# Performance work log

Hardware: AMD Instinct MI355X
Metric: run time of the kernel (lower is better)

Reference implementation:

```python
import jax, jax.numpy as jnp
import numpy as np


def setup_inputs() -> dict:
    key = jax.random.key(0)
    k1, k2, k3, k4, k5 = jax.random.split(key, 5)
    B, S, D = 16, 1024, 64
    query = jax.random.normal(k1, (B, S, D), dtype=jnp.float32)
    key_t = jax.random.normal(k2, (B, S, D), dtype=jnp.float32)
    value = jax.random.normal(k3, (B, S, D), dtype=jnp.float32)
    t_m = jax.random.uniform(k4, (B, S, S), dtype=jnp.float32)
    g_m = jax.random.uniform(k5, (B, S, S), dtype=jnp.float32)
    # causal mask [S, S]: 1 where attention allowed
    mask = jnp.tril(jnp.ones((S, S), dtype=jnp.int32))
    return {"query": query, "key": key_t, "value": value,
            "t_m": t_m, "g_m": g_m, "mask": mask}


def _bias(m):
    # per-batch max over all S*S entries, then abs difference
    mx = jnp.max(m.reshape(m.shape[0], -1), axis=1)  # [B]
    return jnp.abs(m - mx[:, None, None])            # [B, S, S]


def reference(query, key, value, t_m, g_m, mask):
    d_k = query.shape[-1]
    # NOTE: source divides by d_k, not sqrt(d_k)
    scores = jnp.einsum('bqd,bkd->bqk', query, key) / d_k  # [B, S, S]
    scores = scores + _bias(t_m) + _bias(g_m)
    scores = jnp.where(mask[None, :, :] == 0, jnp.float32(-1e9), scores)
    p_attn = jax.nn.softmax(scores, axis=-1)
    return jnp.einsum('bqk,bkd->bqd', p_attn, value)
```

## Files before the change

### kernel.cpp

```cpp
#include <hip/hip_runtime.h>

#define B_  16
#define S_  1024
#define D_  64

typedef __attribute__((ext_vector_type(8))) short bf16x8;
typedef __attribute__((ext_vector_type(4))) float f32x4;

__device__ __forceinline__ unsigned short f2bf(float f) {
    unsigned u = __float_as_uint(f);
    u += 0x7FFF + ((u >> 16) & 1);
    return (unsigned short)(u >> 16);
}

__global__ __launch_bounds__(256, 4) void attn_mfma_kernel(
    const float* __restrict__ Q, const float* __restrict__ K,
    const float* __restrict__ V, const float* __restrict__ t_m,
    const float* __restrict__ g_m, float* __restrict__ out)
{
    __shared__ __align__(16) char smem[17920];
    unsigned short (*s_p)[136] = (unsigned short (*)[136])smem;
    float* cmb = (float*)smem;
    float* cml = (float*)(smem + 17408);

    const int bid = blockIdx.x;
    const int b   = bid & 15;
    const int g   = bid >> 4;
    const int qt  = (g < 32) ? (63 - g) : (g - 32);
    const int qb  = qt << 4;
    const int tid = threadIdx.x;
    const int w   = tid >> 6;
    const int ln  = tid & 63;
    const int lg  = ln >> 4;
    const int lm  = ln & 15;

    const size_t kvb   = (size_t)(b * S_) * D_;
    const size_t biasb = (size_t)b * S_ * S_;
    const float* Kb = K + kvb;
    const float* Vb = V + kvb;

    bf16x8 qa[2];
    #pragma unroll
    for (int ks = 0; ks < 2; ++ks) {
        const float* qp = Q + ((size_t)(b * S_) + qb + lm) * D_ + 32 * ks + 8 * lg;
        const float4 x = *(const float4*)qp;
        const float4 y = *(const float4*)(qp + 4);
        bf16x8 f;
        f[0] = (short)f2bf(x.x); f[1] = (short)f2bf(x.y);
        f[2] = (short)f2bf(x.z); f[3] = (short)f2bf(x.w);
        f[4] = (short)f2bf(y.x); f[5] = (short)f2bf(y.y);
        f[6] = (short)f2bf(y.z); f[7] = (short)f2bf(y.w);
        qa[ks] = f;
    }

    float mrun[4] = {-1e30f, -1e30f, -1e30f, -1e30f};
    float lrun[4] = {0.f, 0.f, 0.f, 0.f};
    const f32x4 z4 = {0.f, 0.f, 0.f, 0.f};
    f32x4 oacc[4] = {z4, z4, z4, z4};

    const int ntw = ((qb + 15 - 32 * w) >> 7) + 1;

    for (int t = 0; t < ntw; ++t) {
        const int ke = (t << 7) + 32 * w;

        bf16x8 kf[2][2];
        #pragma unroll
        for (int nf = 0; nf < 2; ++nf)
            #pragma unroll
            for (int ks = 0; ks < 2; ++ks) {
                const float* kp = Kb + (size_t)(ke + 16 * nf + lm) * D_ + 32 * ks + 8 * lg;
                const float4 x = *(const float4*)kp;
                const float4 y = *(const float4*)(kp + 4);
                bf16x8 f;
                f[0] = (short)f2bf(x.x); f[1] = (short)f2bf(x.y);
                f[2] = (short)f2bf(x.z); f[3] = (short)f2bf(x.w);
                f[4] = (short)f2bf(y.x); f[5] = (short)f2bf(y.y);
                f[6] = (short)f2bf(y.z); f[7] = (short)f2bf(y.w);
                kf[nf][ks] = f;
            }

        float bt[2][4], bg[2][4];
        #pragma unroll
        for (int nf = 0; nf < 2; ++nf)
            #pragma unroll
            for (int r = 0; r < 4; ++r) {
                const size_t off = biasb + (size_t)(qb + 4 * lg + r) * S_
                                 + ke + 16 * nf + lm;
                bt[nf][r] = t_m[off];
                bg[nf][r] = g_m[off];
            }

        f32x4 sa[2] = {z4, z4};
        #pragma unroll
        for (int nf = 0; nf < 2; ++nf)
            #pragma unroll
            for (int ks = 0; ks < 2; ++ks)
                sa[nf] = __builtin_amdgcn_mfma_f32_16x16x32_bf16(
                    qa[ks], kf[nf][ks], sa[nf], 0, 0, 0);

        float vf[4][8];
        #pragma unroll
        for (int nd = 0; nd < 4; ++nd)
            #pragma unroll
            for (int j = 0; j < 8; ++j)
                vf[nd][j] = Vb[(size_t)(ke + 8 * lg + j) * D_ + 16 * nd + lm];

        float p[2][4], tmax[4];
        #pragma unroll
        for (int r = 0; r < 4; ++r) {
            const int qg = qb + 4 * lg + r;
            float s0 = sa[0][r] * (1.f / 64.f) - bt[0][r] - bg[0][r];
            float s1 = sa[1][r] * (1.f / 64.f) - bt[1][r] - bg[1][r];
            if (ke + lm > qg)      s0 = -1e30f;
            if (ke + 16 + lm > qg) s1 = -1e30f;
            p[0][r] = s0;  p[1][r] = s1;
            tmax[r] = fmaxf(s0, s1);
        }
        #pragma unroll
        for (int off = 1; off < 16; off <<= 1)
            #pragma unroll
            for (int r = 0; r < 4; ++r)
                tmax[r] = fmaxf(tmax[r], __shfl_xor(tmax[r], off, 64));

        float a[4];
        #pragma unroll
        for (int r = 0; r < 4; ++r) {
            const float mn = fmaxf(mrun[r], tmax[r]);
            a[r] = __expf(mrun[r] - mn);
            mrun[r] = mn;
            const float p0 = __expf(p[0][r] - mn);
            const float p1 = __expf(p[1][r] - mn);
            p[0][r] = p0;  p[1][r] = p1;
            float rs = p0 + p1;
            #pragma unroll
            for (int off = 1; off < 16; off <<= 1)
                rs += __shfl_xor(rs, off, 64);
            lrun[r] = lrun[r] * a[r] + rs;
        }
        #pragma unroll
        for (int nd = 0; nd < 4; ++nd)
            #pragma unroll
            for (int r = 0; r < 4; ++r)
                oacc[nd][r] *= a[r];

        #pragma unroll
        for (int nf = 0; nf < 2; ++nf)
            #pragma unroll
            for (int r = 0; r < 4; ++r)
                s_p[4 * lg + r][32 * w + 16 * nf + lm] = f2bf(p[nf][r]);
        asm volatile("s_waitcnt lgkmcnt(0)" ::: "memory");
        const bf16x8 pa = *(const bf16x8*)&s_p[lm][32 * w + 8 * lg];

        #pragma unroll
        for (int nd = 0; nd < 4; ++nd) {
            bf16x8 vb;
            #pragma unroll
            for (int j = 0; j < 8; ++j)
                vb[j] = (short)f2bf(vf[nd][j]);
            oacc[nd] = __builtin_amdgcn_mfma_f32_16x16x32_bf16(
                pa, vb, oacc[nd], 0, 0, 0);
        }
    }

    __syncthreads();
    #pragma unroll
    for (int nd = 0; nd < 4; ++nd)
        #pragma unroll
        for (int r = 0; r < 4; ++r)
            cmb[(w * 16 + 4 * lg + r) * 68 + 16 * nd + lm] = oacc[nd][r];
    if (lm == 0) {
        #pragma unroll
        for (int r = 0; r < 4; ++r) {
            cml[w * 32 + 4 * lg + r]      = mrun[r];
            cml[w * 32 + 16 + 4 * lg + r] = lrun[r];
        }
    }
    __syncthreads();
    {
        const int q = tid >> 4, c = tid & 15;
        float mm[4], sc[4];
        float ms = -1e30f;
        #pragma unroll
        for (int i = 0; i < 4; ++i) { mm[i] = cml[i * 32 + q]; ms = fmaxf(ms, mm[i]); }
        float lt = 0.f;
        #pragma unroll
        for (int i = 0; i < 4; ++i) {
            sc[i] = __expf(mm[i] - ms);
            lt += cml[i * 32 + 16 + q] * sc[i];
        }
        const float inv = 1.f / lt;
        float4 acc = make_float4(0.f, 0.f, 0.f, 0.f);
        #pragma unroll
        for (int i = 0; i < 4; ++i) {
            const float4 v = *(const float4*)&cmb[(i * 16 + q) * 68 + 4 * c];
            acc.x += v.x * sc[i];  acc.y += v.y * sc[i];
            acc.z += v.z * sc[i];  acc.w += v.w * sc[i];
        }
        acc.x *= inv; acc.y *= inv; acc.z *= inv; acc.w *= inv;
        *(float4*)(out + ((size_t)(b * S_) + qb + q) * D_ + 4 * c) = acc;
    }
}

extern "C" void kernel_launch(void* const* d_in, const int* in_sizes, int n_in,
                              void* d_out, int out_size, void* d_ws, size_t ws_size,
                              hipStream_t stream) {
    const float* Q   = (const float*)d_in[0];
    const float* Kp  = (const float*)d_in[1];
    const float* V   = (const float*)d_in[2];
    const float* t_m = (const float*)d_in[3];
    const float* g_m = (const float*)d_in[4];

    attn_mfma_kernel<<<1024, 256, 0, stream>>>(Q, Kp, V, t_m, g_m,
                                               (float*)d_out);
}
```

Measured before the change: 35.58 us.

## Split each query tile's key range across eight waves instead of four

Doubles the block size to 512 threads so eight waves share a 16-row query tile. Each wave now strides over keys in steps of 256, which halves the serial loop length per wave. The shared-memory merge of per-wave softmax partials is widened to eight partials, and the output write becomes float2 per thread. The bf16 conversion is also swapped to the library intrinsic. The risks are the heavier cross-wave merge and a tight launch-bounds hint (512 threads, 8 blocks) that may force register spills.

```diff
diff --git a/kernel.cpp b/kernel.cpp
--- a/kernel.cpp
+++ b/kernel.cpp
@@ -1,4 +1,5 @@
 #include <hip/hip_runtime.h>
+#include <hip/hip_bf16.h>
 
 #define B_  16
 #define S_  1024
@@ -7,21 +8,20 @@
 typedef __attribute__((ext_vector_type(8))) short bf16x8;
 typedef __attribute__((ext_vector_type(4))) float f32x4;
 
-__device__ __forceinline__ unsigned short f2bf(float f) {
-    unsigned u = __float_as_uint(f);
-    u += 0x7FFF + ((u >> 16) & 1);
-    return (unsigned short)(u >> 16);
+__device__ __forceinline__ short f2bf(float f) {
+    __hip_bfloat16 h = __float2bfloat16(f);
+    return __builtin_bit_cast(short, h);
 }
 
-__global__ __launch_bounds__(256, 4) void attn_mfma_kernel(
+__global__ __launch_bounds__(512, 8) void attn_mfma_kernel(
     const float* __restrict__ Q, const float* __restrict__ K,
     const float* __restrict__ V, const float* __restrict__ t_m,
     const float* __restrict__ g_m, float* __restrict__ out)
 {
-    __shared__ __align__(16) char smem[17920];
-    unsigned short (*s_p)[136] = (unsigned short (*)[136])smem;
+    __shared__ __align__(16) char smem[35840];
+    unsigned short (*s_p)[264] = (unsigned short (*)[264])smem;
     float* cmb = (float*)smem;
-    float* cml = (float*)(smem + 17408);
+    float* cml = (float*)(smem + 34816);
 
     const int bid = blockIdx.x;
     const int b   = bid & 15;
@@ -46,10 +46,10 @@
         const float4 x = *(const float4*)qp;
         const float4 y = *(const float4*)(qp + 4);
         bf16x8 f;
-        f[0] = (short)f2bf(x.x); f[1] = (short)f2bf(x.y);
-        f[2] = (short)f2bf(x.z); f[3] = (short)f2bf(x.w);
-        f[4] = (short)f2bf(y.x); f[5] = (short)f2bf(y.y);
-        f[6] = (short)f2bf(y.z); f[7] = (short)f2bf(y.w);
+        f[0] = f2bf(x.x); f[1] = f2bf(x.y);
+        f[2] = f2bf(x.z); f[3] = f2bf(x.w);
+        f[4] = f2bf(y.x); f[5] = f2bf(y.y);
+        f[6] = f2bf(y.z); f[7] = f2bf(y.w);
         qa[ks] = f;
     }
 
@@ -58,10 +58,10 @@
     const f32x4 z4 = {0.f, 0.f, 0.f, 0.f};
     f32x4 oacc[4] = {z4, z4, z4, z4};
 
-    const int ntw = ((qb + 15 - 32 * w) >> 7) + 1;
+    const int ntw = ((qb + 15 - 32 * w) >> 8) + 1;
 
     for (int t = 0; t < ntw; ++t) {
-        const int ke = (t << 7) + 32 * w;
+        const int ke = (t << 8) + 32 * w;
 
         bf16x8 kf[2][2];
         #pragma unroll
@@ -72,10 +72,10 @@
                 const float4 x = *(const float4*)kp;
                 const float4 y = *(const float4*)(kp + 4);
                 bf16x8 f;
-                f[0] = (short)f2bf(x.x); f[1] = (short)f2bf(x.y);
-                f[2] = (short)f2bf(x.z); f[3] = (short)f2bf(x.w);
-                f[4] = (short)f2bf(y.x); f[5] = (short)f2bf(y.y);
-                f[6] = (short)f2bf(y.z); f[7] = (short)f2bf(y.w);
+                f[0] = f2bf(x.x); f[1] = f2bf(x.y);
+                f[2] = f2bf(x.z); f[3] = f2bf(x.w);
+                f[4] = f2bf(y.x); f[5] = f2bf(y.y);
+                f[6] = f2bf(y.z); f[7] = f2bf(y.w);
                 kf[nf][ks] = f;
             }
 
@@ -147,7 +147,7 @@
         for (int nf = 0; nf < 2; ++nf)
             #pragma unroll
             for (int r = 0; r < 4; ++r)
-                s_p[4 * lg + r][32 * w + 16 * nf + lm] = f2bf(p[nf][r]);
+                s_p[4 * lg + r][32 * w + 16 * nf + lm] = (unsigned short)f2bf(p[nf][r]);
         asm volatile("s_waitcnt lgkmcnt(0)" ::: "memory");
         const bf16x8 pa = *(const bf16x8*)&s_p[lm][32 * w + 8 * lg];
 
@@ -156,7 +156,7 @@
             bf16x8 vb;
             #pragma unroll
             for (int j = 0; j < 8; ++j)
-                vb[j] = (short)f2bf(vf[nd][j]);
+                vb[j] = f2bf(vf[nd][j]);
             oacc[nd] = __builtin_amdgcn_mfma_f32_16x16x32_bf16(
                 pa, vb, oacc[nd], 0, 0, 0);
         }
@@ -177,27 +177,26 @@
     }
     __syncthreads();
     {
-        const int q = tid >> 4, c = tid & 15;
-        float mm[4], sc[4];
+        const int q = tid >> 5, c = tid & 31;
+        float mm[8], sc[8];
         float ms = -1e30f;
         #pragma unroll
-        for (int i = 0; i < 4; ++i) { mm[i] = cml[i * 32 + q]; ms = fmaxf(ms, mm[i]); }
+        for (int i = 0; i < 8; ++i) { mm[i] = cml[i * 32 + q]; ms = fmaxf(ms, mm[i]); }
         float lt = 0.f;
         #pragma unroll
-        for (int i = 0; i < 4; ++i) {
+        for (int i = 0; i < 8; ++i) {
             sc[i] = __expf(mm[i] - ms);
             lt += cml[i * 32 + 16 + q] * sc[i];
         }
         const float inv = 1.f / lt;
-        float4 acc = make_float4(0.f, 0.f, 0.f, 0.f);
-        #pragma unroll
-        for (int i = 0; i < 4; ++i) {
-            const float4 v = *(const float4*)&cmb[(i * 16 + q) * 68 + 4 * c];
+        float2 acc = make_float2(0.f, 0.f);
+        #pragma unroll
+        for (int i = 0; i < 8; ++i) {
+            const float2 v = *(const float2*)&cmb[(i * 16 + q) * 68 + 2 * c];
             acc.x += v.x * sc[i];  acc.y += v.y * sc[i];
-            acc.z += v.z * sc[i];  acc.w += v.w * sc[i];
-        }
-        acc.x *= inv; acc.y *= inv; acc.z *= inv; acc.w *= inv;
-        *(float4*)(out + ((size_t)(b * S_) + qb + q) * D_ + 4 * c) = acc;
+        }
+        acc.x *= inv; acc.y *= inv;
+        *(float2*)(out + ((size_t)(b * S_) + qb + q) * D_ + 2 * c) = acc;
     }
 }
 
@@ -210,6 +209,6 @@
     const float* t_m = (const float*)d_in[3];
     const float* g_m = (const float*)d_in[4];
 
-    attn_mfma_kernel<<<1024, 256, 0, stream>>>(Q, Kp, V, t_m, g_m,
+    attn_mfma_kernel<<<1024, 512, 0, stream>>>(Q, Kp, V, t_m, g_m,
                                                (float*)d_out);
 }
```

Result: slower. 102.7 us (+188.8%).

## Pre-convert K to bf16 and transpose V in a prep kernel

Applied to the files above, without the earlier changes.

Adds a prep kernel that converts K to bf16 and writes V transposed as bf16 into the workspace. The attention kernel then loads K and V fragments as single 16-byte vectors instead of doing per-element float loads and bf16 conversions in the inner loop. This removes the 32 strided scalar V loads per thread per tile and the repeated conversion work. In exchange it adds a second launch and an extra round trip through the workspace. The original kernel is kept as a fallback when the workspace is too small.

```diff
diff --git a/kernel.cpp b/kernel.cpp
--- a/kernel.cpp
+++ b/kernel.cpp
@@ -1,4 +1,5 @@
 #include <hip/hip_runtime.h>
+#include <hip/hip_bf16.h>
 
 #define B_  16
 #define S_  1024
@@ -7,15 +8,44 @@
 typedef __attribute__((ext_vector_type(8))) short bf16x8;
 typedef __attribute__((ext_vector_type(4))) float f32x4;
 
-__device__ __forceinline__ unsigned short f2bf(float f) {
-    unsigned u = __float_as_uint(f);
-    u += 0x7FFF + ((u >> 16) & 1);
-    return (unsigned short)(u >> 16);
-}
-
-__global__ __launch_bounds__(256, 4) void attn_mfma_kernel(
-    const float* __restrict__ Q, const float* __restrict__ K,
-    const float* __restrict__ V, const float* __restrict__ t_m,
+__device__ __forceinline__ unsigned short f2bf_u(float f) {
+    __hip_bfloat16 h = __float2bfloat16(f);
+    return __builtin_bit_cast(unsigned short, h);
+}
+__device__ __forceinline__ short f2bf(float f) {
+    return (short)f2bf_u(f);
+}
+__device__ __forceinline__ unsigned pk2(float a, float b) {
+    return (unsigned)f2bf_u(a) | ((unsigned)f2bf_u(b) << 16);
+}
+
+__global__ __launch_bounds__(256) void prep_kernel(
+    const float* __restrict__ K, const float* __restrict__ V,
+    unsigned short* __restrict__ Kbf, unsigned short* __restrict__ VT)
+{
+    const int bid = blockIdx.x;
+    if (bid < 512) {
+        const size_t i = ((size_t)bid * 256 + threadIdx.x) * 8;
+        const float4 x = *(const float4*)(K + i);
+        const float4 y = *(const float4*)(K + i + 4);
+        uint4 o = { pk2(x.x, x.y), pk2(x.z, x.w), pk2(y.x, y.y), pk2(y.z, y.w) };
+        *(uint4*)(Kbf + i) = o;
+    } else {
+        const int i  = (bid - 512) * 256 + threadIdx.x;
+        const int d  = i & 63;
+        const int kg = (i >> 6) & 127;
+        const int b  = i >> 13;
+        const float* vp = V + ((size_t)b * S_ + (size_t)kg * 8) * D_ + d;
+        const float v0 = vp[0],   v1 = vp[64],  v2 = vp[128], v3 = vp[192];
+        const float v4 = vp[256], v5 = vp[320], v6 = vp[384], v7 = vp[448];
+        uint4 o = { pk2(v0, v1), pk2(v2, v3), pk2(v4, v5), pk2(v6, v7) };
+        *(uint4*)(VT + ((size_t)b * D_ + d) * S_ + kg * 8) = o;
+    }
+}
+
+__global__ __launch_bounds__(256, 4) void attn_mfma_pre(
+    const unsigned short* __restrict__ Kbf, const unsigned short* __restrict__ VT,
+    const float* __restrict__ Q, const float* __restrict__ t_m,
     const float* __restrict__ g_m, float* __restrict__ out)
 {
     __shared__ __align__(16) char smem[17920];
@@ -34,10 +64,15 @@
     const int lg  = ln >> 4;
     const int lm  = ln & 15;
 
-    const size_t kvb   = (size_t)(b * S_) * D_;
     const size_t biasb = (size_t)b * S_ * S_;
-    const float* Kb = K + kvb;
-    const float* Vb = V + kvb;
+    const float* tmb = t_m + biasb + (size_t)(qb + 4 * lg) * S_ + lm;
+    const float* gmb = g_m + biasb + (size_t)(qb + 4 * lg) * S_ + lm;
+
+    const unsigned short* Kbb = Kbf + ((size_t)(b * S_) + lm) * D_ + 8 * lg;
+    const unsigned short* vt0 = VT + ((size_t)(b * D_) + 0  + lm) * S_ + 8 * lg;
+    const unsigned short* vt1 = VT + ((size_t)(b * D_) + 16 + lm) * S_ + 8 * lg;
+    const unsigned short* vt2 = VT + ((size_t)(b * D_) + 32 + lm) * S_ + 8 * lg;
+    const unsigned short* vt3 = VT + ((size_t)(b * D_) + 48 + lm) * S_ + 8 * lg;
 
     bf16x8 qa[2];
     #pragma unroll
@@ -46,10 +81,10 @@
         const float4 x = *(const float4*)qp;
         const float4 y = *(const float4*)(qp + 4);
         bf16x8 f;
-        f[0] = (short)f2bf(x.x); f[1] = (short)f2bf(x.y);
-        f[2] = (short)f2bf(x.z); f[3] = (short)f2bf(x.w);
-        f[4] = (short)f2bf(y.x); f[5] = (short)f2bf(y.y);
-        f[6] = (short)f2bf(y.z); f[7] = (short)f2bf(y.w);
+        f[0] = f2bf(x.x); f[1] = f2bf(x.y);
+        f[2] = f2bf(x.z); f[3] = f2bf(x.w);
+        f[4] = f2bf(y.x); f[5] = f2bf(y.y);
+        f[6] = f2bf(y.z); f[7] = f2bf(y.w);
         qa[ks] = f;
     }
 
@@ -63,47 +98,32 @@
     for (int t = 0; t < ntw; ++t) {
         const int ke = (t << 7) + 32 * w;
 
-        bf16x8 kf[2][2];
-        #pragma unroll
-        for (int nf = 0; nf < 2; ++nf)
-            #pragma unroll
-            for (int ks = 0; ks < 2; ++ks) {
-                const float* kp = Kb + (size_t)(ke + 16 * nf + lm) * D_ + 32 * ks + 8 * lg;
-                const float4 x = *(const float4*)kp;
-                const float4 y = *(const float4*)(kp + 4);
-                bf16x8 f;
-                f[0] = (short)f2bf(x.x); f[1] = (short)f2bf(x.y);
-                f[2] = (short)f2bf(x.z); f[3] = (short)f2bf(x.w);
-                f[4] = (short)f2bf(y.x); f[5] = (short)f2bf(y.y);
-                f[6] = (short)f2bf(y.z); f[7] = (short)f2bf(y.w);
-                kf[nf][ks] = f;
+        const bf16x8* kp = (const bf16x8*)(Kbb + (size_t)ke * D_);
+        bf16x8 kf00 = kp[0];
+        bf16x8 kf01 = *(const bf16x8*)((const unsigned short*)kp + 32);
+        bf16x8 kf10 = *(const bf16x8*)((const unsigned short*)kp + 16 * D_);
+        bf16x8 kf11 = *(const bf16x8*)((const unsigned short*)kp + 16 * D_ + 32);
+
+        const bf16x8 vb0 = *(const bf16x8*)(vt0 + ke);
+        const bf16x8 vb1 = *(const bf16x8*)(vt1 + ke);
+        const bf16x8 vb2 = *(const bf16x8*)(vt2 + ke);
+        const bf16x8 vb3 = *(const bf16x8*)(vt3 + ke);
+
+        float bt[2][4], bg[2][4];
+        #pragma unroll
+        for (int nf = 0; nf < 2; ++nf)
+            #pragma unroll
+            for (int r = 0; r < 4; ++r) {
+                const size_t off = (size_t)r * S_ + ke + 16 * nf;
+                bt[nf][r] = tmb[off];
+                bg[nf][r] = gmb[off];
             }
 
-        float bt[2][4], bg[2][4];
-        #pragma unroll
-        for (int nf = 0; nf < 2; ++nf)
-            #pragma unroll
-            for (int r = 0; r < 4; ++r) {
-                const size_t off = biasb + (size_t)(qb + 4 * lg + r) * S_
-                                 + ke + 16 * nf + lm;
-                bt[nf][r] = t_m[off];
-                bg[nf][r] = g_m[off];
-            }
-
         f32x4 sa[2] = {z4, z4};
-        #pragma unroll
-        for (int nf = 0; nf < 2; ++nf)
-            #pragma unroll
-            for (int ks = 0; ks < 2; ++ks)
-                sa[nf] = __builtin_amdgcn_mfma_f32_16x16x32_bf16(
-                    qa[ks], kf[nf][ks], sa[nf], 0, 0, 0);
-
-        float vf[4][8];
-        #pragma unroll
-        for (int nd = 0; nd < 4; ++nd)
-            #pragma unroll
-            for (int j = 0; j < 8; ++j)
-                vf[nd][j] = Vb[(size_t)(ke + 8 * lg + j) * D_ + 16 * nd + lm];
+        sa[0] = __builtin_amdgcn_mfma_f32_16x16x32_bf16(qa[0], kf00, sa[0], 0, 0, 0);
+        sa[0] = __builtin_amdgcn_mfma_f32_16x16x32_bf16(qa[1], kf01, sa[0], 0, 0, 0);
+        sa[1] = __builtin_amdgcn_mfma_f32_16x16x32_bf16(qa[0], kf10, sa[1], 0, 0, 0);
+        sa[1] = __builtin_amdgcn_mfma_f32_16x16x32_bf16(qa[1], kf11, sa[1], 0, 0, 0);
 
         float p[2][4], tmax[4];
         #pragma unroll
@@ -122,11 +142,10 @@
             for (int r = 0; r < 4; ++r)
                 tmax[r] = fmaxf(tmax[r], __shfl_xor(tmax[r], off, 64));
 
-        float a[4];
         #pragma unroll
         for (int r = 0; r < 4; ++r) {
             const float mn = fmaxf(mrun[r], tmax[r]);
-            a[r] = __expf(mrun[r] - mn);
+            const float a  = __expf(mrun[r] - mn);
             mrun[r] = mn;
             const float p0 = __expf(p[0][r] - mn);
             const float p1 = __expf(p[1][r] - mn);
@@ -135,28 +154,203 @@
             #pragma unroll
             for (int off = 1; off < 16; off <<= 1)
                 rs += __shfl_xor(rs, off, 64);
-            lrun[r] = lrun[r] * a[r] + rs;
-        }
-        #pragma unroll
-        for (int nd = 0; nd < 4; ++nd)
+            lrun[r] = lrun[r] * a + rs;
+            #pragma unroll
+            for (int nd = 0; nd < 4; ++nd) oacc[nd][r] *= a;
+        }
+
+        #pragma unroll
+        for (int nf = 0; nf < 2; ++nf)
             #pragma unroll
             for (int r = 0; r < 4; ++r)
-                oacc[nd][r] *= a[r];
-
-        #pragma unroll
-        for (int nf = 0; nf < 2; ++nf)
-            #pragma unroll
-            for (int r = 0; r < 4; ++r)
-                s_p[4 * lg + r][32 * w + 16 * nf + lm] = f2bf(p[nf][r]);
+                s_p[4 * lg + r][32 * w + 16 * nf + lm] = f2bf_u(p[nf][r]);
         asm volatile("s_waitcnt lgkmcnt(0)" ::: "memory");
         const bf16x8 pa = *(const bf16x8*)&s_p[lm][32 * w + 8 * lg];
 
+        oacc[0] = __builtin_amdgcn_mfma_f32_16x16x32_bf16(pa, vb0, oacc[0], 0, 0, 0);
+        oacc[1] = __builtin_amdgcn_mfma_f32_16x16x32_bf16(pa, vb1, oacc[1], 0, 0, 0);
+        oacc[2] = __builtin_amdgcn_mfma_f32_16x16x32_bf16(pa, vb2, oacc[2], 0, 0, 0);
+        oacc[3] = __builtin_amdgcn_mfma_f32_16x16x32_bf16(pa, vb3, oacc[3], 0, 0, 0);
+    }
+
+    __syncthreads();
+    #pragma unroll
+    for (int nd = 0; nd < 4; ++nd)
+        #pragma unroll
+        for (int r = 0; r < 4; ++r)
+            cmb[(w * 16 + 4 * lg + r) * 68 + 16 * nd + lm] = oacc[nd][r];
+    if (lm == 0) {
+        #pragma unroll
+        for (int r = 0; r < 4; ++r) {
+            cml[w * 32 + 4 * lg + r]      = mrun[r];
+            cml[w * 32 + 16 + 4 * lg + r] = lrun[r];
+        }
+    }
+    __syncthreads();
+    {
+        const int q = tid >> 4, c = tid & 15;
+        float mm[4], sc[4];
+        float ms = -1e30f;
+        #pragma unroll
+        for (int i = 0; i < 4; ++i) { mm[i] = cml[i * 32 + q]; ms = fmaxf(ms, mm[i]); }
+        float lt = 0.f;
+        #pragma unroll
+        for (int i = 0; i < 4; ++i) {
+            sc[i] = __expf(mm[i] - ms);
+            lt += cml[i * 32 + 16 + q] * sc[i];
+        }
+        const float inv = 1.f / lt;
+        float4 acc = make_float4(0.f, 0.f, 0.f, 0.f);
+        #pragma unroll
+        for (int i = 0; i < 4; ++i) {
+            const float4 v = *(const float4*)&cmb[(i * 16 + q) * 68 + 4 * c];
+            acc.x += v.x * sc[i];  acc.y += v.y * sc[i];
+            acc.z += v.z * sc[i];  acc.w += v.w * sc[i];
+        }
+        acc.x *= inv; acc.y *= inv; acc.z *= inv; acc.w *= inv;
+        *(float4*)(out + ((size_t)(b * S_) + qb + q) * D_ + 4 * c) = acc;
+    }
+}
+
+__global__ __launch_bounds__(256, 4) void attn_mfma_kernel(
+    const float* __restrict__ Q, const float* __restrict__ K,
+    const float* __restrict__ V, const float* __restrict__ t_m,
+    const float* __restrict__ g_m, float* __restrict__ out)
+{
+    __shared__ __align__(16) char smem[17920];
+    unsigned short (*s_p)[136] = (unsigned short (*)[136])smem;
+    float* cmb = (float*)smem;
+    float* cml = (float*)(smem + 17408);
+
+    const int bid = blockIdx.x;
+    const int b   = bid & 15;
+    const int g   = bid >> 4;
+    const int qt  = (g < 32) ? (63 - g) : (g - 32);
+    const int qb  = qt << 4;
+    const int tid = threadIdx.x;
+    const int w   = tid >> 6;
+    const int ln  = tid & 63;
+    const int lg  = ln >> 4;
+    const int lm  = ln & 15;
+
+    const size_t kvb   = (size_t)(b * S_) * D_;
+    const size_t biasb = (size_t)b * S_ * S_;
+    const float* Kb = K + kvb;
+    const float* Vb = V + kvb;
+
+    bf16x8 qa[2];
+    #pragma unroll
+    for (int ks = 0; ks < 2; ++ks) {
+        const float* qp = Q + ((size_t)(b * S_) + qb + lm) * D_ + 32 * ks + 8 * lg;
+        const float4 x = *(const float4*)qp;
+        const float4 y = *(const float4*)(qp + 4);
+        bf16x8 f;
+        f[0] = f2bf(x.x); f[1] = f2bf(x.y);
+        f[2] = f2bf(x.z); f[3] = f2bf(x.w);
+        f[4] = f2bf(y.x); f[5] = f2bf(y.y);
+        f[6] = f2bf(y.z); f[7] = f2bf(y.w);
+        qa[ks] = f;
+    }
+
+    float mrun[4] = {-1e30f, -1e30f, -1e30f, -1e30f};
+    float lrun[4] = {0.f, 0.f, 0.f, 0.f};
+    const f32x4 z4 = {0.f, 0.f, 0.f, 0.f};
+    f32x4 oacc[4] = {z4, z4, z4, z4};
+
+    const int ntw = ((qb + 15 - 32 * w) >> 7) + 1;
+
+    for (int t = 0; t < ntw; ++t) {
+        const int ke = (t << 7) + 32 * w;
+
+        bf16x8 kf[2][2];
+        #pragma unroll
+        for (int nf = 0; nf < 2; ++nf)
+            #pragma unroll
+            for (int ks = 0; ks < 2; ++ks) {
+                const float* kp = Kb + (size_t)(ke + 16 * nf + lm) * D_ + 32 * ks + 8 * lg;
+                const float4 x = *(const float4*)kp;
+                const float4 y = *(const float4*)(kp + 4);
+                bf16x8 f;
+                f[0] = f2bf(x.x); f[1] = f2bf(x.y);
+                f[2] = f2bf(x.z); f[3] = f2bf(x.w);
+                f[4] = f2bf(y.x); f[5] = f2bf(y.y);
+                f[6] = f2bf(y.z); f[7] = f2bf(y.w);
+                kf[nf][ks] = f;
+            }
+
+        float bt[2][4], bg[2][4];
+        #pragma unroll
+        for (int nf = 0; nf < 2; ++nf)
+            #pragma unroll
+            for (int r = 0; r < 4; ++r) {
+                const size_t off = biasb + (size_t)(qb + 4 * lg + r) * S_
+                                 + ke + 16 * nf + lm;
+                bt[nf][r] = t_m[off];
+                bg[nf][r] = g_m[off];
+            }
+
+        f32x4 sa[2] = {z4, z4};
+        #pragma unroll
+        for (int nf = 0; nf < 2; ++nf)
+            #pragma unroll
+            for (int ks = 0; ks < 2; ++ks)
+                sa[nf] = __builtin_amdgcn_mfma_f32_16x16x32_bf16(
+                    qa[ks], kf[nf][ks], sa[nf], 0, 0, 0);
+
+        float vf[4][8];
+        #pragma unroll
+        for (int nd = 0; nd < 4; ++nd)
+            #pragma unroll
+            for (int j = 0; j < 8; ++j)
+                vf[nd][j] = Vb[(size_t)(ke + 8 * lg + j) * D_ + 16 * nd + lm];
+
+        float p[2][4], tmax[4];
+        #pragma unroll
+        for (int r = 0; r < 4; ++r) {
+            const int qg = qb + 4 * lg + r;
+            float s0 = sa[0][r] * (1.f / 64.f) - bt[0][r] - bg[0][r];
+            float s1 = sa[1][r] * (1.f / 64.f) - bt[1][r] - bg[1][r];
+            if (ke + lm > qg)      s0 = -1e30f;
+            if (ke + 16 + lm > qg) s1 = -1e30f;
+            p[0][r] = s0;  p[1][r] = s1;
+            tmax[r] = fmaxf(s0, s1);
+        }
+        #pragma unroll
+        for (int off = 1; off < 16; off <<= 1)
+            #pragma unroll
+            for (int r = 0; r < 4; ++r)
+                tmax[r] = fmaxf(tmax[r], __shfl_xor(tmax[r], off, 64));
+
+        #pragma unroll
+        for (int r = 0; r < 4; ++r) {
+            const float mn = fmaxf(mrun[r], tmax[r]);
+            const float a  = __expf(mrun[r] - mn);
+            mrun[r] = mn;
+            const float p0 = __expf(p[0][r] - mn);
+            const float p1 = __expf(p[1][r] - mn);
+            p[0][r] = p0;  p[1][r] = p1;
+            float rs = p0 + p1;
+            #pragma unroll
+            for (int off = 1; off < 16; off <<= 1)
+                rs += __shfl_xor(rs, off, 64);
+            lrun[r] = lrun[r] * a + rs;
+            #pragma unroll
+            for (int nd = 0; nd < 4; ++nd) oacc[nd][r] *= a;
+        }
+
+        #pragma unroll
+        for (int nf = 0; nf < 2; ++nf)
+            #pragma unroll
+            for (int r = 0; r < 4; ++r)
+                s_p[4 * lg + r][32 * w + 16 * nf + lm] = f2bf_u(p[nf][r]);
+        asm volatile("s_waitcnt lgkmcnt(0)" ::: "memory");
+        const bf16x8 pa = *(const bf16x8*)&s_p[lm][32 * w + 8 * lg];
+
         #pragma unroll
         for (int nd = 0; nd < 4; ++nd) {
             bf16x8 vb;
             #pragma unroll
-            for (int j = 0; j < 8; ++j)
-                vb[j] = (short)f2bf(vf[nd][j]);
+            for (int j = 0; j < 8; ++j) vb[j] = f2bf(vf[nd][j]);
             oacc[nd] = __builtin_amdgcn_mfma_f32_16x16x32_bf16(
                 pa, vb, oacc[nd], 0, 0, 0);
         }
@@ -210,6 +404,15 @@
     const float* t_m = (const float*)d_in[3];
     const float* g_m = (const float*)d_in[4];
 
-    attn_mfma_kernel<<<1024, 256, 0, stream>>>(Q, Kp, V, t_m, g_m,
-                                               (float*)d_out);
-}
+    const size_t need = (size_t)2 * B_ * S_ * D_ * sizeof(unsigned short);
+    if (ws_size >= need) {
+        unsigned short* Kbf = (unsigned short*)d_ws;
+        unsigned short* VT  = Kbf + (size_t)B_ * S_ * D_;
+        prep_kernel<<<1024, 256, 0, stream>>>(Kp, V, Kbf, VT);
+        attn_mfma_pre<<<1024, 256, 0, stream>>>(Kbf, VT, Q, t_m, g_m,
+                                                (float*)d_out);
+    } else {
+        attn_mfma_kernel<<<1024, 256, 0, stream>>>(Q, Kp, V, t_m, g_m,
+                                                   (float*)d_out);
+    }
+}
```

Result: faster. 34.24 us (-3.8%).
